# Kernel tuning notes

Measured on AMD Instinct MI355X. Metric: run time of the kernel, lower is better.

The kernel has to match this reference:

```python
import jax, jax.numpy as jnp
import numpy as np

B, T, D = 2, 2048, 2048
H = 16
SEM_HD, GEO_HD = 64, 64
SEM_D, GEO_D = H * SEM_HD, H * GEO_HD  # 1024, 1024
V_D = 2048
V_HD = V_D // H  # 128
ROPE_BASE = 10000.0
NEG_INF = -1e9


def _shape(x, hd):
    # (B, T, H*hd) -> (B, H, T, hd)
    b, t, _ = x.shape
    return x.reshape(b, t, H, hd).transpose(0, 2, 1, 3)


def _rope(x, pos_offset=0):
    # half-split (Llama-style) rotary on last dim; x: (B, H, T, hd)
    hd = x.shape[-1]
    half = hd // 2
    inv_freq = 1.0 / (ROPE_BASE ** (jnp.arange(0, half, dtype=jnp.float32) / half))
    pos = jnp.arange(x.shape[2], dtype=jnp.float32) + pos_offset
    ang = pos[:, None] * inv_freq[None, :]            # (T, half)
    cos, sin = jnp.cos(ang), jnp.sin(ang)
    x1, x2 = x[..., :half], x[..., half:]
    return jnp.concatenate([x1 * cos - x2 * sin, x2 * cos + x1 * sin], axis=-1).astype(x.dtype)


def setup_inputs() -> dict:
    key = jax.random.key(0)
    ks = jax.random.split(key, 9)
    s = lambda fan_in: 1.0 / np.sqrt(fan_in)
    return {
        "x": jax.random.normal(ks[0], (B, T, D), dtype=jnp.float32),
        "w_q_sem": jax.random.normal(ks[1], (D, SEM_D), dtype=jnp.float32) * s(D),
        "w_k_sem": jax.random.normal(ks[2], (D, SEM_D), dtype=jnp.float32) * s(D),
        "w_q_geo": jax.random.normal(ks[3], (D, GEO_D), dtype=jnp.float32) * s(D),
        "w_k_geo": jax.random.normal(ks[4], (D, GEO_D), dtype=jnp.float32) * s(D),
        "w_v": jax.random.normal(ks[5], (D, V_D), dtype=jnp.float32) * s(D),
        "w_out": jax.random.normal(ks[6], (V_D, D), dtype=jnp.float32) * s(V_D),
        "gate_logit": jax.random.normal(ks[7], (H,), dtype=jnp.float32) * 0.1,
        "gate_w": jax.random.normal(ks[8], (D, H), dtype=jnp.float32) * 0.01,
    }


def reference(x, w_q_sem, w_k_sem, w_q_geo, w_k_geo, w_v, w_out, gate_logit, gate_w):
    sem_scale = 1.0 / np.sqrt(float(SEM_HD))
    geo_scale = 1.0 / np.sqrt(float(GEO_HD))

    qs = _shape(x @ w_q_sem, SEM_HD)   # (B,H,T,sem_hd)
    ks = _shape(x @ w_k_sem, SEM_HD)
    qg = _shape(x @ w_q_geo, GEO_HD)   # (B,H,T,geo_hd)
    kg = _shape(x @ w_k_geo, GEO_HD)
    vh = _shape(x @ w_v, V_HD)         # (B,H,T,v_hd)

    # RoPE only on geometric dims
    qg = _rope(qg)
    kg = _rope(kg)

    sem_scores = jnp.einsum("bhtd,bhsd->bhts", qs, ks) * sem_scale
    geo_scores = jnp.einsum("bhtd,bhsd->bhts", qg, kg) * geo_scale

    # per-head gate: static logit + dynamic projection of x, sigmoid in fp32
    dyn = (x @ gate_w).transpose(0, 2, 1)[..., None]            # (B,H,T,1)
    gate = jax.nn.sigmoid(gate_logit[None, :, None, None] + dyn)
    scores = gate * sem_scores + (1.0 - gate) * geo_scores      # (B,H,T,S)

    causal = jnp.tril(jnp.ones((T, T), dtype=bool))
    scores = jnp.where(causal[None, None], scores, NEG_INF)
    attn = jax.nn.softmax(scores, axis=-1)

    out = jnp.einsum("bhts,bhsd->bhtd", attn, vh)               # (B,H,T,v_hd)
    y = out.transpose(0, 2, 1, 3).reshape(B, T, V_D) @ w_out    # (B,T,D)
    return y
```

## Files before the change

kernel.cpp:

```cpp
#include <hip/hip_runtime.h>
#include <hip/hip_bf16.h>
#include <math.h>

#define B_ 2
#define T_ 2048
#define D_ 2048
#define H_ 16

typedef __attribute__((ext_vector_type(8))) short bf16x8;
typedef __attribute__((ext_vector_type(4))) float f32x4;
typedef unsigned short ushort_t;

__device__ __forceinline__ ushort_t f2bf(float f) {
    unsigned int u = __float_as_uint(f);
    u += 0x7fffu + ((u >> 16) & 1u);
    return (ushort_t)(u >> 16);
}

__device__ __forceinline__ void gl_lds16(const void* g, void* l) {
    __builtin_amdgcn_global_load_lds(
        (const __attribute__((address_space(1))) void*)g,
        (__attribute__((address_space(3))) void*)l, 16, 0, 0);
}

__global__ __launch_bounds__(256) void cvt_bf16(
    const float* __restrict__ in, ushort_t* __restrict__ out)
{
    const int base = (blockIdx.x * 256 + threadIdx.x) * 8;
    const float4 a = *(const float4*)(in + base);
    const float4 b = *(const float4*)(in + base + 4);
    unsigned int r0 = (unsigned int)f2bf(a.x) | ((unsigned int)f2bf(a.y) << 16);
    unsigned int r1 = (unsigned int)f2bf(a.z) | ((unsigned int)f2bf(a.w) << 16);
    unsigned int r2 = (unsigned int)f2bf(b.x) | ((unsigned int)f2bf(b.y) << 16);
    unsigned int r3 = (unsigned int)f2bf(b.z) | ((unsigned int)f2bf(b.w) << 16);
    *(uint4*)(out + base) = make_uint4(r0, r1, r2, r3);
}

__global__ __launch_bounds__(256) void cvt_tr_bf16(
    const float* __restrict__ in, ushort_t* __restrict__ out, int K, int N)
{
    __shared__ float t[64][65];
    const int n0 = blockIdx.x * 64, k0 = blockIdx.y * 64;
    const int tx = threadIdx.x & 63, ty = threadIdx.x >> 6;
#pragma unroll
    for (int i = 0; i < 16; i++) {
        const int r = i * 4 + ty;
        t[r][tx] = in[(size_t)(k0 + r) * N + n0 + tx];
    }
    __syncthreads();
#pragma unroll
    for (int i = 0; i < 16; i++) {
        const int nn = i * 4 + ty;
        out[(size_t)(n0 + nn) * K + k0 + tx] = f2bf(t[tx][nn]);
    }
}

__global__ __launch_bounds__(256) void gemm_bf16_bt(
    const ushort_t* __restrict__ Ab, const ushort_t* __restrict__ BTb,
    float* __restrict__ C, int M, int N, int K)
{
    __shared__ ushort_t As[4096];
    __shared__ ushort_t Bs[4096];

    const int tid = threadIdx.x;
    const int w = tid >> 6, lane = tid & 63;
    const int wr = w >> 1, wc = w & 1;
    const int row0 = blockIdx.y << 7, col0 = blockIdx.x << 7;
    const int lm = lane & 15, lk = (lane >> 4) << 3;

    f32x4 acc[4][4];
#pragma unroll
    for (int m = 0; m < 4; m++)
#pragma unroll
        for (int n = 0; n < 4; n++) {
            acc[m][n][0] = 0.f; acc[m][n][1] = 0.f;
            acc[m][n][2] = 0.f; acc[m][n][3] = 0.f;
        }

    for (int k0 = 0; k0 < K; k0 += 32) {
        __syncthreads();
#pragma unroll
        for (int i = 0; i < 2; i++) {
            const int chunk = i * 4 + w;
            const int idx = chunk * 64 + lane;
            const int r = idx >> 2;
            const int c = (idx & 3) << 3;
            gl_lds16(Ab + (size_t)(row0 + r) * K + k0 + c, As + chunk * 512);
            gl_lds16(BTb + (size_t)(col0 + r) * K + k0 + c, Bs + chunk * 512);
        }
        __syncthreads();

        bf16x8 av[4], bv[4];
#pragma unroll
        for (int m = 0; m < 4; m++)
            av[m] = *(const bf16x8*)&As[(wr * 64 + m * 16 + lm) * 32 + lk];
#pragma unroll
        for (int n = 0; n < 4; n++)
            bv[n] = *(const bf16x8*)&Bs[(wc * 64 + n * 16 + lm) * 32 + lk];
#pragma unroll
        for (int m = 0; m < 4; m++)
#pragma unroll
            for (int n = 0; n < 4; n++)
                acc[m][n] = __builtin_amdgcn_mfma_f32_16x16x32_bf16(
                    av[m], bv[n], acc[m][n], 0, 0, 0);
    }

#pragma unroll
    for (int m = 0; m < 4; m++) {
        const int rowb = row0 + wr * 64 + m * 16 + ((lane >> 4) << 2);
#pragma unroll
        for (int n = 0; n < 4; n++) {
            const int col = col0 + wc * 64 + n * 16 + lm;
#pragma unroll
            for (int r = 0; r < 4; r++)
                C[(size_t)(rowb + r) * N + col] = acc[m][n][r];
        }
    }
}

__global__ __launch_bounds__(256) void gate_kernel(
    const float* __restrict__ x, const float* __restrict__ gw,
    const float* __restrict__ glogit, float* __restrict__ gate)
{
    __shared__ float xs[2048];
    __shared__ float red[256];
    const int row = blockIdx.x, tid = threadIdx.x;
#pragma unroll
    for (int i = 0; i < 8; i++) xs[i * 256 + tid] = x[(size_t)row * 2048 + i * 256 + tid];
    __syncthreads();
    const int h = tid & 15, chunk = tid >> 4;
    float acc = 0.f;
#pragma unroll 4
    for (int d0 = 0; d0 < 128; d0++) {
        const int d = chunk * 128 + d0;
        acc += xs[d] * gw[d * 16 + h];
    }
    red[tid] = acc;
    __syncthreads();
    for (int st = 8; st >= 1; st >>= 1) {
        if (chunk < st) red[chunk * 16 + h] += red[(chunk + st) * 16 + h];
        __syncthreads();
    }
    if (tid < 16) gate[row * 16 + tid] = 1.f / (1.f + expf(-(glogit[tid] + red[tid])));
}

__global__ __launch_bounds__(256) void rope_table(float2* __restrict__ tab)
{
    const int gid = blockIdx.x * 256 + threadIdx.x;
    const int j = gid & 31, t = gid >> 5;
    const float invf = exp2f((float)j * -0.41524101186091903f);
    const float ang = (float)t * invf;
    tab[gid] = make_float2(cosf(ang), sinf(ang));
}

__global__ __launch_bounds__(256) void prep_qk(
    const float* __restrict__ QK, const float* __restrict__ GATE,
    const float2* __restrict__ tab,
    ushort_t* __restrict__ Qb, ushort_t* __restrict__ Kb)
{
    const int gid = blockIdx.x * 256 + threadIdx.x;
    const int j = gid & 31;
    const int h = (gid >> 5) & 15;
    const int row = gid >> 9;
    const int t = row & (T_ - 1);
    const int b = row >> 11;

    const float* base = QK + (size_t)row * 4096 + h * 64 + j;
    const float qs1 = base[0],    qs2 = base[32];
    const float ks1 = base[1024], ks2 = base[1056];
    const float qg1 = base[2048], qg2 = base[2080];
    const float kg1 = base[3072], kg2 = base[3104];

    const float g = GATE[row * 16 + h];
    const float scs = g * 0.125f, scg = (1.f - g) * 0.125f;
    const float2 cs = tab[t * 32 + j];
    const float c = cs.x, s = cs.y;

    const float qo1 = (qg1 * c - qg2 * s) * scg;
    const float qo2 = (qg2 * c + qg1 * s) * scg;
    const float ko1 = kg1 * c - kg2 * s;
    const float ko2 = kg2 * c + kg1 * s;

    const size_t obase = ((size_t)(b * 16 + h) * 2048 + t) * 128;
    Qb[obase + j]       = f2bf(qs1 * scs);
    Qb[obase + j + 32]  = f2bf(qs2 * scs);
    Qb[obase + 64 + j]  = f2bf(qo1);
    Qb[obase + 96 + j]  = f2bf(qo2);
    const int sw = (t & 7) << 3;
    Kb[obase + (j ^ sw)]        = f2bf(ks1);
    Kb[obase + ((j + 32) ^ sw)] = f2bf(ks2);
    Kb[obase + ((64 + j) ^ sw)] = f2bf(ko1);
    Kb[obase + ((96 + j) ^ sw)] = f2bf(ko2);
}

__global__ __launch_bounds__(256) void prep_v(
    const float* __restrict__ Vb, ushort_t* __restrict__ Vt)
{
    __shared__ float tile[64][65];
    const int t0 = blockIdx.x * 64, dv0 = blockIdx.y * 64, bh = blockIdx.z;
    const int b = bh >> 4, h = bh & 15;
    const int c = threadIdx.x & 63, rq = threadIdx.x >> 6;
#pragma unroll
    for (int i = 0; i < 16; i++) {
        const int r = i * 4 + rq;
        tile[r][c] = Vb[(size_t)(b * T_ + t0 + r) * 2048 + h * 128 + dv0 + c];
    }
    __syncthreads();
#pragma unroll
    for (int i = 0; i < 16; i++) {
        const int dvr = i * 4 + rq;
        const int dv = dv0 + dvr;
        Vt[((size_t)bh * 128 + dv) * 2048 + t0 + (c ^ ((dv & 7) << 3))] = f2bf(tile[c][dvr]);
    }
}

__global__ __launch_bounds__(256, 2) void attn_mfma(
    const ushort_t* __restrict__ Qb, const ushort_t* __restrict__ Kb,
    const ushort_t* __restrict__ Vt, ushort_t* __restrict__ OUT)
{
    __shared__ ushort_t Ks[64 * 128];
    __shared__ ushort_t Vs[128 * 64];
    __shared__ ushort_t Ps[4][32 * 72];

    const int tid = threadIdx.x;
    const int w = tid >> 6, l = tid & 63;
    const int lg = l >> 4, lm = l & 15;
    const int bh = blockIdx.y;
    const int t0 = blockIdx.x << 7;
    const size_t hb = (size_t)bh * 2048 * 128;

    bf16x8 qf[2][4];
#pragma unroll
    for (int m = 0; m < 2; m++)
#pragma unroll
        for (int ks = 0; ks < 4; ks++)
            qf[m][ks] = *(const bf16x8*)(Qb + hb +
                (size_t)(t0 + w * 32 + m * 16 + lm) * 128 + ks * 32 + lg * 8);

    f32x4 o[2][8];
    float mi[2][4], li[2][4];
#pragma unroll
    for (int m = 0; m < 2; m++) {
#pragma unroll
        for (int r = 0; r < 4; r++) { mi[m][r] = -1e30f; li[m][r] = 0.f; }
#pragma unroll
        for (int nv = 0; nv < 8; nv++) {
            o[m][nv][0] = 0.f; o[m][nv][1] = 0.f; o[m][nv][2] = 0.f; o[m][nv][3] = 0.f;
        }
    }

    ushort_t* pw = &Ps[w][0];
    const int nkt = (t0 >> 6) + 2;

    for (int kt = 0; kt < nkt; kt++) {
        const int s0 = kt << 6;
        __syncthreads();
#pragma unroll
        for (int rr = 0; rr < 4; rr++) {
            const int chunk = rr * 4 + w;
            gl_lds16(Kb + hb + (size_t)(s0 + chunk * 4 + lg) * 128 + lm * 8,
                     Ks + chunk * 512);
        }
#pragma unroll
        for (int rr = 0; rr < 4; rr++) {
            const int chunk = rr * 4 + w;
            gl_lds16(Vt + hb + (size_t)(chunk * 8 + (l >> 3)) * 2048 + s0 + (l & 7) * 8,
                     Vs + chunk * 512);
        }
        __syncthreads();

        f32x4 sacc[2][4];
#pragma unroll
        for (int m = 0; m < 2; m++)
#pragma unroll
            for (int n = 0; n < 4; n++) {
                sacc[m][n][0] = 0.f; sacc[m][n][1] = 0.f;
                sacc[m][n][2] = 0.f; sacc[m][n][3] = 0.f;
            }
#pragma unroll
        for (int ks = 0; ks < 4; ks++) {
            bf16x8 bfr[4];
#pragma unroll
            for (int n = 0; n < 4; n++) {
                const int key = n * 16 + lm;
                const int d = ks * 32 + lg * 8;
                bfr[n] = *(const bf16x8*)&Ks[key * 128 + (d ^ ((key & 7) << 3))];
            }
#pragma unroll
            for (int m = 0; m < 2; m++)
#pragma unroll
                for (int n = 0; n < 4; n++)
                    sacc[m][n] = __builtin_amdgcn_mfma_f32_16x16x32_bf16(
                        qf[m][ks], bfr[n], sacc[m][n], 0, 0, 0);
        }

        if (kt >= nkt - 2) {
#pragma unroll
            for (int m = 0; m < 2; m++)
#pragma unroll
                for (int n = 0; n < 4; n++)
#pragma unroll
                    for (int r = 0; r < 4; r++) {
                        const int rowt = t0 + w * 32 + m * 16 + lg * 4 + r;
                        const int colt = s0 + n * 16 + lm;
                        if (colt > rowt) sacc[m][n][r] = -1e30f;
                    }
        }

#pragma unroll
        for (int m = 0; m < 2; m++) {
#pragma unroll
            for (int r = 0; r < 4; r++) {
                float mt = fmaxf(fmaxf(sacc[0 + m][0][r], sacc[m][1][r]),
                                 fmaxf(sacc[m][2][r], sacc[m][3][r]));
                mt = fmaxf(mt, __shfl_xor(mt, 1));
                mt = fmaxf(mt, __shfl_xor(mt, 2));
                mt = fmaxf(mt, __shfl_xor(mt, 4));
                mt = fmaxf(mt, __shfl_xor(mt, 8));
                const float mnew = fmaxf(mi[m][r], mt);
                const float alpha = __expf(mi[m][r] - mnew);
                float rs = 0.f;
#pragma unroll
                for (int n = 0; n < 4; n++) {
                    const float p = __expf(sacc[m][n][r] - mnew);
                    sacc[m][n][r] = p;
                    rs += p;
                }
                rs += __shfl_xor(rs, 1);
                rs += __shfl_xor(rs, 2);
                rs += __shfl_xor(rs, 4);
                rs += __shfl_xor(rs, 8);
                li[m][r] = li[m][r] * alpha + rs;
                mi[m][r] = mnew;
#pragma unroll
                for (int nv = 0; nv < 8; nv++) o[m][nv][r] *= alpha;
#pragma unroll
                for (int n = 0; n < 4; n++)
                    pw[(m * 16 + lg * 4 + r) * 72 + n * 16 + lm] = f2bf(sacc[m][n][r]);
            }
        }

#pragma unroll
        for (int ks2 = 0; ks2 < 2; ks2++) {
            bf16x8 pa[2];
#pragma unroll
            for (int m = 0; m < 2; m++)
                pa[m] = *(const bf16x8*)&pw[(m * 16 + lm) * 72 + ks2 * 32 + lg * 8];
#pragma unroll
            for (int nv = 0; nv < 8; nv++) {
                const int dv = nv * 16 + lm;
                const bf16x8 vb = *(const bf16x8*)&Vs[dv * 64 +
                    ((ks2 * 32 + lg * 8) ^ ((dv & 7) << 3))];
#pragma unroll
                for (int m = 0; m < 2; m++)
                    o[m][nv] = __builtin_amdgcn_mfma_f32_16x16x32_bf16(
                        pa[m], vb, o[m][nv], 0, 0, 0);
            }
        }
    }

    const int b = bh >> 4, h = bh & 15;
#pragma unroll
    for (int m = 0; m < 2; m++)
#pragma unroll
        for (int r = 0; r < 4; r++) {
            const float inv = 1.f / li[m][r];
            const int trow = t0 + w * 32 + m * 16 + lg * 4 + r;
            ushort_t* orow = OUT + (size_t)(b * T_ + trow) * 2048 + h * 128 + lm;
#pragma unroll
            for (int nv = 0; nv < 8; nv++)
                orow[nv * 16] = f2bf(o[m][nv][r] * inv);
        }
}

extern "C" void kernel_launch(void* const* d_in, const int* in_sizes, int n_in,
                              void* d_out, int out_size, void* d_ws, size_t ws_size,
                              hipStream_t stream)
{
    const float* x       = (const float*)d_in[0];
    const float* w_q_sem = (const float*)d_in[1];
    const float* w_k_sem = (const float*)d_in[2];
    const float* w_q_geo = (const float*)d_in[3];
    const float* w_k_geo = (const float*)d_in[4];
    const float* w_v     = (const float*)d_in[5];
    const float* w_out   = (const float*)d_in[6];
    const float* glogit  = (const float*)d_in[7];
    const float* gw      = (const float*)d_in[8];
    float* out = (float*)d_out;

    const int M = B_ * T_;
    float* ws = (float*)d_ws;

    float* QK   = ws;
    float* Vb   = QK + (size_t)16 * 1024 * 1024;
    float* GATE = Vb + (size_t)8 * 1024 * 1024;
    ushort_t* WT  = (ushort_t*)(GATE + 65536);
    ushort_t* xbf = WT + (size_t)8 * 1024 * 1024;
    ushort_t* Qb  = xbf + (size_t)8 * 1024 * 1024;
    float2* ROPETAB = (float2*)(Qb + (size_t)8 * 1024 * 1024);
    ushort_t* Kb  = xbf;
    ushort_t* Vt  = WT;
    ushort_t* ATTbf = (ushort_t*)QK;

    dim3 blk(256);

    cvt_bf16<<<dim3(M * 2048 / (256 * 8)), blk, 0, stream>>>(x, xbf);
    cvt_tr_bf16<<<dim3(16, 32), blk, 0, stream>>>(w_q_sem, WT + (size_t)0 * 2097152, 2048, 1024);
    cvt_tr_bf16<<<dim3(16, 32), blk, 0, stream>>>(w_k_sem, WT + (size_t)1 * 2097152, 2048, 1024);
    cvt_tr_bf16<<<dim3(16, 32), blk, 0, stream>>>(w_q_geo, WT + (size_t)2 * 2097152, 2048, 1024);
    cvt_tr_bf16<<<dim3(16, 32), blk, 0, stream>>>(w_k_geo, WT + (size_t)3 * 2097152, 2048, 1024);
    gemm_bf16_bt<<<dim3(32, 32), blk, 0, stream>>>(xbf, WT, QK, M, 4096, 2048);
    cvt_tr_bf16<<<dim3(32, 32), blk, 0, stream>>>(w_v, WT, 2048, 2048);
    gemm_bf16_bt<<<dim3(16, 32), blk, 0, stream>>>(xbf, WT, Vb, M, 2048, 2048);

    gate_kernel<<<dim3(M), blk, 0, stream>>>(x, gw, glogit, GATE);
    rope_table<<<dim3(256), blk, 0, stream>>>(ROPETAB);
    prep_qk<<<dim3(M * 16 * 32 / 256), blk, 0, stream>>>(QK, GATE, ROPETAB, Qb, Kb);
    prep_v<<<dim3(T_ / 64, 2, 32), blk, 0, stream>>>(Vb, Vt);

    attn_mfma<<<dim3(T_ / 128, 32), blk, 0, stream>>>(Qb, Kb, Vt, ATTbf);

    cvt_tr_bf16<<<dim3(32, 32), blk, 0, stream>>>(w_out, WT, 2048, 2048);
    gemm_bf16_bt<<<dim3(16, 32), blk, 0, stream>>>(ATTbf, WT, out, M, 2048, 2048);
}
```

Measured before the change: 555.5 us.

## Fuse QK projection epilogue with gate/RoPE, bf16 V output, XCD tile remap

The QK projection GEMM now applies gate scaling, RoPE and the swizzled bf16 layout in its epilogue, so the fp32 QK intermediate and the separate prep_qk pass are gone. The V GEMM writes bf16 directly, which halves the bytes prep_v reads. A tile remap groups neighbouring tiles onto the same XCD for L2 reuse, and attention blocks launch in reverse order so the longest causal tiles start first. The epilogue's strided scattered bf16 stores may coalesce poorly.

After: 552.2 us. About the same (-0.6%).

```diff
diff --git a/kernel.cpp b/kernel.cpp
--- a/kernel.cpp
+++ b/kernel.cpp
@@ -55,20 +55,13 @@
     }
 }
 
-__global__ __launch_bounds__(256) void gemm_bf16_bt(
+__device__ __forceinline__ void gemm_core(
     const ushort_t* __restrict__ Ab, const ushort_t* __restrict__ BTb,
-    float* __restrict__ C, int M, int N, int K)
-{
-    __shared__ ushort_t As[4096];
-    __shared__ ushort_t Bs[4096];
-
-    const int tid = threadIdx.x;
-    const int w = tid >> 6, lane = tid & 63;
+    int K, int row0, int col0,
+    ushort_t* As, ushort_t* Bs, f32x4 (&acc)[4][4], int w, int lane)
+{
+    const int lm = lane & 15, lk = (lane >> 4) << 3;
     const int wr = w >> 1, wc = w & 1;
-    const int row0 = blockIdx.y << 7, col0 = blockIdx.x << 7;
-    const int lm = lane & 15, lk = (lane >> 4) << 3;
-
-    f32x4 acc[4][4];
 #pragma unroll
     for (int m = 0; m < 4; m++)
 #pragma unroll
@@ -104,7 +97,32 @@
                 acc[m][n] = __builtin_amdgcn_mfma_f32_16x16x32_bf16(
                     av[m], bv[n], acc[m][n], 0, 0, 0);
     }
-
+}
+
+__device__ __forceinline__ void xcd_tile(int& row0, int& col0)
+{
+    const int o = blockIdx.y * gridDim.x + blockIdx.x;
+    const int nwg = gridDim.x * gridDim.y;
+    const int s = (o & 7) * (nwg >> 3) + (o >> 3);
+    col0 = (s % gridDim.x) << 7;
+    row0 = (s / gridDim.x) << 7;
+}
+
+__global__ __launch_bounds__(256) void gemm_bf16_bt(
+    const ushort_t* __restrict__ Ab, const ushort_t* __restrict__ BTb,
+    float* __restrict__ C, int N, int K)
+{
+    __shared__ ushort_t As[4096];
+    __shared__ ushort_t Bs[4096];
+    const int tid = threadIdx.x;
+    const int w = tid >> 6, lane = tid & 63;
+    int row0, col0;
+    xcd_tile(row0, col0);
+    f32x4 acc[4][4];
+    gemm_core(Ab, BTb, K, row0, col0, As, Bs, acc, w, lane);
+
+    const int wr = w >> 1, wc = w & 1;
+    const int lm = lane & 15;
 #pragma unroll
     for (int m = 0; m < 4; m++) {
         const int rowb = row0 + wr * 64 + m * 16 + ((lane >> 4) << 2);
@@ -114,6 +132,98 @@
 #pragma unroll
             for (int r = 0; r < 4; r++)
                 C[(size_t)(rowb + r) * N + col] = acc[m][n][r];
+        }
+    }
+}
+
+__global__ __launch_bounds__(256) void gemm_bf16_bf16out(
+    const ushort_t* __restrict__ Ab, const ushort_t* __restrict__ BTb,
+    ushort_t* __restrict__ C, int N, int K)
+{
+    __shared__ ushort_t As[4096];
+    __shared__ ushort_t Bs[4096];
+    const int tid = threadIdx.x;
+    const int w = tid >> 6, lane = tid & 63;
+    int row0, col0;
+    xcd_tile(row0, col0);
+    f32x4 acc[4][4];
+    gemm_core(Ab, BTb, K, row0, col0, As, Bs, acc, w, lane);
+
+    const int wr = w >> 1, wc = w & 1;
+    const int lm = lane & 15;
+#pragma unroll
+    for (int m = 0; m < 4; m++) {
+        const int rowb = row0 + wr * 64 + m * 16 + ((lane >> 4) << 2);
+#pragma unroll
+        for (int n = 0; n < 4; n++) {
+            const int col = col0 + wc * 64 + n * 16 + lm;
+#pragma unroll
+            for (int r = 0; r < 4; r++)
+                C[(size_t)(rowb + r) * N + col] = f2bf(acc[m][n][r]);
+        }
+    }
+}
+
+__global__ __launch_bounds__(256) void gemm_qk_fused(
+    const ushort_t* __restrict__ Ab, const ushort_t* __restrict__ BTb,
+    const float* __restrict__ GATE, const float2* __restrict__ tab,
+    ushort_t* __restrict__ Qb, ushort_t* __restrict__ Kb, int K)
+{
+    __shared__ ushort_t As[4096];
+    __shared__ ushort_t Bs[4096];
+    const int tid = threadIdx.x;
+    const int w = tid >> 6, lane = tid & 63;
+    int row0, col0;
+    xcd_tile(row0, col0);
+    f32x4 acc[4][4];
+    gemm_core(Ab, BTb, K, row0, col0, As, Bs, acc, w, lane);
+
+    const int wr = w >> 1, wc = w & 1;
+    const int lm = lane & 15, lg = lane >> 4;
+    const int col_base = col0 + wc * 64;
+    const int region = col_base >> 10;
+    const int h = (col_base >> 6) & 15;
+
+#pragma unroll
+    for (int m = 0; m < 4; m++) {
+        const int rbase = row0 + wr * 64 + m * 16 + (lg << 2);
+#pragma unroll
+        for (int r = 0; r < 4; r++) {
+            const int row = rbase + r;
+            const int t = row & (T_ - 1);
+            const int bq = row >> 11;
+            const size_t obase = ((size_t)(bq * 16 + h) * 2048 + t) * 128;
+            if (region == 0) {
+                const float sc = GATE[row * 16 + h] * 0.125f;
+#pragma unroll
+                for (int n = 0; n < 4; n++)
+                    Qb[obase + n * 16 + lm] = f2bf(acc[m][n][r] * sc);
+            } else if (region == 1) {
+                const int sw = (t & 7) << 3;
+#pragma unroll
+                for (int n = 0; n < 4; n++)
+                    Kb[obase + ((n * 16 + lm) ^ sw)] = f2bf(acc[m][n][r]);
+            } else if (region == 2) {
+                const float sc = (1.f - GATE[row * 16 + h]) * 0.125f;
+#pragma unroll
+                for (int n = 0; n < 2; n++) {
+                    const int j = n * 16 + lm;
+                    const float2 cs = tab[t * 32 + j];
+                    const float x1 = acc[m][n][r], x2 = acc[m][n + 2][r];
+                    Qb[obase + 64 + j] = f2bf((x1 * cs.x - x2 * cs.y) * sc);
+                    Qb[obase + 96 + j] = f2bf((x2 * cs.x + x1 * cs.y) * sc);
+                }
+            } else {
+                const int sw = (t & 7) << 3;
+#pragma unroll
+                for (int n = 0; n < 2; n++) {
+                    const int j = n * 16 + lm;
+                    const float2 cs = tab[t * 32 + j];
+                    const float x1 = acc[m][n][r], x2 = acc[m][n + 2][r];
+                    Kb[obase + ((64 + j) ^ sw)] = f2bf(x1 * cs.x - x2 * cs.y);
+                    Kb[obase + ((96 + j) ^ sw)] = f2bf(x2 * cs.x + x1 * cs.y);
+                }
+            }
         }
     }
 }
@@ -153,64 +263,24 @@
     tab[gid] = make_float2(cosf(ang), sinf(ang));
 }
 
-__global__ __launch_bounds__(256) void prep_qk(
-    const float* __restrict__ QK, const float* __restrict__ GATE,
-    const float2* __restrict__ tab,
-    ushort_t* __restrict__ Qb, ushort_t* __restrict__ Kb)
-{
-    const int gid = blockIdx.x * 256 + threadIdx.x;
-    const int j = gid & 31;
-    const int h = (gid >> 5) & 15;
-    const int row = gid >> 9;
-    const int t = row & (T_ - 1);
-    const int b = row >> 11;
-
-    const float* base = QK + (size_t)row * 4096 + h * 64 + j;
-    const float qs1 = base[0],    qs2 = base[32];
-    const float ks1 = base[1024], ks2 = base[1056];
-    const float qg1 = base[2048], qg2 = base[2080];
-    const float kg1 = base[3072], kg2 = base[3104];
-
-    const float g = GATE[row * 16 + h];
-    const float scs = g * 0.125f, scg = (1.f - g) * 0.125f;
-    const float2 cs = tab[t * 32 + j];
-    const float c = cs.x, s = cs.y;
-
-    const float qo1 = (qg1 * c - qg2 * s) * scg;
-    const float qo2 = (qg2 * c + qg1 * s) * scg;
-    const float ko1 = kg1 * c - kg2 * s;
-    const float ko2 = kg2 * c + kg1 * s;
-
-    const size_t obase = ((size_t)(b * 16 + h) * 2048 + t) * 128;
-    Qb[obase + j]       = f2bf(qs1 * scs);
-    Qb[obase + j + 32]  = f2bf(qs2 * scs);
-    Qb[obase + 64 + j]  = f2bf(qo1);
-    Qb[obase + 96 + j]  = f2bf(qo2);
-    const int sw = (t & 7) << 3;
-    Kb[obase + (j ^ sw)]        = f2bf(ks1);
-    Kb[obase + ((j + 32) ^ sw)] = f2bf(ks2);
-    Kb[obase + ((64 + j) ^ sw)] = f2bf(ko1);
-    Kb[obase + ((96 + j) ^ sw)] = f2bf(ko2);
-}
-
 __global__ __launch_bounds__(256) void prep_v(
-    const float* __restrict__ Vb, ushort_t* __restrict__ Vt)
-{
-    __shared__ float tile[64][65];
+    const ushort_t* __restrict__ Vbb, ushort_t* __restrict__ Vt)
+{
+    __shared__ ushort_t tile[64][65];
     const int t0 = blockIdx.x * 64, dv0 = blockIdx.y * 64, bh = blockIdx.z;
     const int b = bh >> 4, h = bh & 15;
     const int c = threadIdx.x & 63, rq = threadIdx.x >> 6;
 #pragma unroll
     for (int i = 0; i < 16; i++) {
         const int r = i * 4 + rq;
-        tile[r][c] = Vb[(size_t)(b * T_ + t0 + r) * 2048 + h * 128 + dv0 + c];
+        tile[r][c] = Vbb[(size_t)(b * T_ + t0 + r) * 2048 + h * 128 + dv0 + c];
     }
     __syncthreads();
 #pragma unroll
     for (int i = 0; i < 16; i++) {
         const int dvr = i * 4 + rq;
         const int dv = dv0 + dvr;
-        Vt[((size_t)bh * 128 + dv) * 2048 + t0 + (c ^ ((dv & 7) << 3))] = f2bf(tile[c][dvr]);
+        Vt[((size_t)bh * 128 + dv) * 2048 + t0 + (c ^ ((dv & 7) << 3))] = tile[c][dvr];
     }
 }
 
@@ -226,7 +296,7 @@
     const int w = tid >> 6, l = tid & 63;
     const int lg = l >> 4, lm = l & 15;
     const int bh = blockIdx.y;
-    const int t0 = blockIdx.x << 7;
+    const int t0 = (gridDim.x - 1 - blockIdx.x) << 7;
     const size_t hb = (size_t)bh * 2048 * 128;
 
     bf16x8 qf[2][4];
@@ -311,7 +381,7 @@
         for (int m = 0; m < 2; m++) {
 #pragma unroll
             for (int r = 0; r < 4; r++) {
-                float mt = fmaxf(fmaxf(sacc[0 + m][0][r], sacc[m][1][r]),
+                float mt = fmaxf(fmaxf(sacc[m][0][r], sacc[m][1][r]),
                                  fmaxf(sacc[m][2][r], sacc[m][3][r]));
                 mt = fmaxf(mt, __shfl_xor(mt, 1));
                 mt = fmaxf(mt, __shfl_xor(mt, 2));
@@ -389,18 +459,17 @@
     float* out = (float*)d_out;
 
     const int M = B_ * T_;
-    float* ws = (float*)d_ws;
-
-    float* QK   = ws;
-    float* Vb   = QK + (size_t)16 * 1024 * 1024;
-    float* GATE = Vb + (size_t)8 * 1024 * 1024;
-    ushort_t* WT  = (ushort_t*)(GATE + 65536);
-    ushort_t* xbf = WT + (size_t)8 * 1024 * 1024;
-    ushort_t* Qb  = xbf + (size_t)8 * 1024 * 1024;
-    float2* ROPETAB = (float2*)(Qb + (size_t)8 * 1024 * 1024);
-    ushort_t* Kb  = xbf;
-    ushort_t* Vt  = WT;
-    ushort_t* ATTbf = (ushort_t*)QK;
+    const size_t MB8 = (size_t)8 * 1024 * 1024;
+
+    ushort_t* xbf = (ushort_t*)d_ws;
+    ushort_t* WT  = xbf + MB8;
+    ushort_t* Qb  = WT + MB8;
+    ushort_t* Kb  = Qb + MB8;
+    ushort_t* Vt  = Kb + MB8;
+    ushort_t* Vbb = Vt + MB8;
+    float* GATE   = (float*)(Vbb + MB8);
+    float2* TAB   = (float2*)(GATE + 65536);
+    ushort_t* ATTbf = Vbb;
 
     dim3 blk(256);
 
@@ -409,17 +478,17 @@
     cvt_tr_bf16<<<dim3(16, 32), blk, 0, stream>>>(w_k_sem, WT + (size_t)1 * 2097152, 2048, 1024);
     cvt_tr_bf16<<<dim3(16, 32), blk, 0, stream>>>(w_q_geo, WT + (size_t)2 * 2097152, 2048, 1024);
     cvt_tr_bf16<<<dim3(16, 32), blk, 0, stream>>>(w_k_geo, WT + (size_t)3 * 2097152, 2048, 1024);
-    gemm_bf16_bt<<<dim3(32, 32), blk, 0, stream>>>(xbf, WT, QK, M, 4096, 2048);
+    gate_kernel<<<dim3(M), blk, 0, stream>>>(x, gw, glogit, GATE);
+    rope_table<<<dim3(256), blk, 0, stream>>>(TAB);
+
+    gemm_qk_fused<<<dim3(32, 32), blk, 0, stream>>>(xbf, WT, GATE, TAB, Qb, Kb, 2048);
+
     cvt_tr_bf16<<<dim3(32, 32), blk, 0, stream>>>(w_v, WT, 2048, 2048);
-    gemm_bf16_bt<<<dim3(16, 32), blk, 0, stream>>>(xbf, WT, Vb, M, 2048, 2048);
-
-    gate_kernel<<<dim3(M), blk, 0, stream>>>(x, gw, glogit, GATE);
-    rope_table<<<dim3(256), blk, 0, stream>>>(ROPETAB);
-    prep_qk<<<dim3(M * 16 * 32 / 256), blk, 0, stream>>>(QK, GATE, ROPETAB, Qb, Kb);
-    prep_v<<<dim3(T_ / 64, 2, 32), blk, 0, stream>>>(Vb, Vt);
+    gemm_bf16_bf16out<<<dim3(16, 32), blk, 0, stream>>>(xbf, WT, Vbb, 2048, 2048);
+    prep_v<<<dim3(T_ / 64, 2, 32), blk, 0, stream>>>(Vbb, Vt);
 
     attn_mfma<<<dim3(T_ / 128, 32), blk, 0, stream>>>(Qb, Kb, Vt, ATTbf);
 
     cvt_tr_bf16<<<dim3(32, 32), blk, 0, stream>>>(w_out, WT, 2048, 2048);
-    gemm_bf16_bt<<<dim3(16, 32), blk, 0, stream>>>(ATTbf, WT, out, M, 2048, 2048);
-}
+    gemm_bf16_bt<<<dim3(16, 32), blk, 0, stream>>>(ATTbf, WT, out, 2048, 2048);
+}
```
